# Optimization experiments

Hardware: AMD Instinct MI355X
Metric: run time of the kernel (lower is better)

## Reference

```python
import jax, jax.numpy as jnp
import numpy as np

N, E, C, MID = 20000, 320000, 16, 32
EPS = 1e-8

# ---- real Clebsch-Gordan (Q_J) matrices for degree pairs up to l=1, real-SH m-order (-l..l) i.e. (y,z,x) for l=1 ----

def _q_matrices():
    Q0 = np.eye(3, dtype=np.float32)[:, :, None] / np.sqrt(3.0)          # 1x1 -> J=0
    eps = np.zeros((3, 3, 3), dtype=np.float32)
    for (a, b, c_) in [(0, 1, 2), (1, 2, 0), (2, 0, 1)]:
        eps[a, b, c_] = 1.0
        eps[a, c_, b] = -1.0
    Q1 = eps / np.sqrt(2.0)                                               # 1x1 -> J=1 (cross product)
    Q2 = np.zeros((3, 3, 5), dtype=np.float32)                            # 1x1 -> J=2 (sym traceless)
    s2 = 1.0 / np.sqrt(2.0); s6 = 1.0 / np.sqrt(6.0)
    Q2[2, 0, 0] = Q2[0, 2, 0] = s2          # ~xy
    Q2[0, 1, 1] = Q2[1, 0, 1] = s2          # ~yz
    Q2[0, 0, 2] = -s6; Q2[1, 1, 2] = 2 * s6; Q2[2, 2, 2] = -s6  # ~(2z2-x2-y2)
    Q2[1, 2, 3] = Q2[2, 1, 3] = s2          # ~xz
    Q2[2, 2, 4] = s2; Q2[0, 0, 4] = -s2     # ~(x2-y2)
    return Q0, Q1, Q2

_Q0, _Q1, _Q2 = _q_matrices()


def _basis(u):
    """u: [E,3] unit edge directions -> basis tensors per (d_in,d_out) pair."""
    x, y, z = u[:, 0], u[:, 1], u[:, 2]
    Ep = u.shape[0]
    Y0 = jnp.full((Ep,), 0.28209479177387814, u.dtype)
    Y1 = 0.4886025119029199 * jnp.stack([y, z, x], -1)                    # m=-1,0,1
    Y2 = jnp.stack([1.0925484305920792 * x * y,
                    1.0925484305920792 * y * z,
                    0.31539156525252005 * (3.0 * z * z - 1.0),
                    1.0925484305920792 * x * z,
                    0.5462742152960396 * (x * x - y * y)], -1)
    b00 = Y0.reshape(Ep, 1, 1, 1, 1, 1)
    b01 = Y1.reshape(Ep, 1, 3, 1, 1, 1)
    b10 = Y1.reshape(Ep, 1, 1, 1, 3, 1)
    K0 = Y0[:, None, None] * jnp.asarray(_Q0[:, :, 0])
    K1 = jnp.einsum('em,abm->eab', Y1, jnp.asarray(_Q1))
    K2 = jnp.einsum('em,abm->eab', Y2, jnp.asarray(_Q2))
    b11 = jnp.stack([K0, K1, K2], -1).reshape(Ep, 1, 3, 1, 3, 3)          # num_freq=3 (J=0,1,2)
    return b00, b01, b10, b11


def _bn(x, g, b):  # BatchNorm1d, training-mode stats over edges, eps=1e-5
    mu = x.mean(0)
    var = ((x - mu) ** 2).mean(0)
    return (x - mu) * jax.lax.rsqrt(var + 1e-5) * g + b


def _hidden(feat, W1, b1, g1, be1, W2, b2, g2, be2):
    h = jax.nn.relu(_bn(feat @ W1 + b1, g1, be1))
    return jax.nn.relu(_bn(h @ W2 + b2, g2, be2))


def _kernel(Rflat, basis, nco, do_dim, nci, di_dim, nf):
    # RadialFunc output view: [E, nc_out, 1, nc_in, 1, num_freq]; contract freq with basis
    R = Rflat.reshape(-1, nco, 1, nci, 1, nf)
    k = (R * basis).sum(-1)                        # [E,nco,do_dim,nci,di_dim]
    return k.reshape(-1, nco * do_dim, nci * di_dim)


def _norm_bias(x, bias):  # GNormBias: relu(|x| + b) * phase
    n = jnp.sqrt((x * x).sum(-1, keepdims=True) + 1e-12)
    phase = x / jnp.maximum(n, EPS)
    return jax.nn.relu(n[..., 0] + bias)[..., None] * phase


def _forward(src, dst, pos, c, v, w,
             rW1, rb1, rg1, rbe1, rW2, rb2, rg2, rbe2,
             w3_a00, b3_a00, w3_a01, b3_a01, w3_a10, b3_a10, w3_a11, b3_a11,
             w3_b01, b3_b01, w3_b11, b3_b11,
             selfA0, selfA1, selfB1, nbias0, nbias1):
    n_nodes = c.shape[0]
    n_edges = src.shape[0]
    rel = pos[dst] - pos[src]
    r = jnp.sqrt((rel * rel).sum(-1, keepdims=True))                      # [E,1]
    u = rel / jnp.maximum(r, EPS)
    b00, b01, b10, b11 = _basis(u)
    feat = jnp.concatenate([w, r], -1)                                    # [E, edge_dim+1]
    # all 6 radial-net hiddens at once: [6,E,MID]
    H = jax.vmap(_hidden, in_axes=(None, 0, 0, 0, 0, 0, 0, 0, 0))(
        feat, rW1, rb1, rg1, rbe1, rW2, rb2, rg2, rbe2)
    deg = jax.ops.segment_sum(jnp.ones((n_edges,), feat.dtype), dst, num_segments=n_nodes)
    inv = (1.0 / jnp.maximum(deg, 1.0))[:, None, None]
    mask = (deg > 0).astype(feat.dtype)[:, None, None]
    # ---- layer A: in {0:1,1:1} -> mid {0:C,1:C} ----
    k00 = _kernel(H[0] @ w3_a00 + b3_a00, b00, C, 1, 1, 1, 1)             # [E,C,1]
    k01 = _kernel(H[1] @ w3_a01 + b3_a01, b01, C, 3, 1, 1, 1)             # [E,3C,1]
    k10 = _kernel(H[2] @ w3_a10 + b3_a10, b10, C, 1, 1, 3, 1)             # [E,C,3]
    k11 = _kernel(H[3] @ w3_a11 + b3_a11, b11, C, 3, 1, 3, 3)             # [E,3C,3]
    s0 = c[src].reshape(n_edges, 1, 1)
    s1 = v[src].reshape(n_edges, 3, 1)
    m0 = (k00 @ s0 + k10 @ s1).reshape(n_edges, C, 1)
    m1 = (k01 @ s0 + k11 @ s1).reshape(n_edges, C, 3)
    h0 = jax.ops.segment_sum(m0, dst, num_segments=n_nodes) * inv \
         + jnp.einsum('oi,nid->nod', selfA0[0], c) * mask
    h1 = jax.ops.segment_sum(m1, dst, num_segments=n_nodes) * inv \
         + jnp.einsum('oi,nid->nod', selfA1[0], v) * mask
    # ---- GNormBias on mid fiber ----
    h0 = _norm_bias(h0, nbias0)
    h1 = _norm_bias(h1, nbias1)
    # ---- layer B: mid {0:C,1:C} -> out {1:2} ----
    kb01 = _kernel(H[4] @ w3_b01 + b3_b01, b01, 2, 3, C, 1, 1)            # [E,6,C]
    kb11 = _kernel(H[5] @ w3_b11 + b3_b11, b11, 2, 3, C, 3, 3)            # [E,6,3C]
    t0 = h0[src]                                                          # [E,C,1]
    t1 = h1[src].reshape(n_edges, C * 3, 1)
    mB = (kb01 @ t0 + kb11 @ t1).reshape(n_edges, 2, 3)
    out = jax.ops.segment_sum(mB, dst, num_segments=n_nodes) * inv \
          + jnp.einsum('oi,nid->nod', selfB1[0], h1) * mask
    return out                                                            # [N,2,3]


def setup_inputs() -> dict:
    key = jax.random.key(0)
    ks = jax.random.split(key, 40)
    def rn(i, shape, scale=1.0):
        return jax.random.normal(ks[i], shape, jnp.float32) * scale
    K = 6
    sc = 1.0 / np.sqrt(MID)
    d = {}
    d['src'] = jax.random.randint(ks[0], (E,), 0, N)
    d['dst'] = jax.random.randint(ks[1], (E,), 0, N)
    d['pos'] = rn(2, (N, 3))
    d['c'] = rn(3, (N, 1, 1))
    d['v'] = rn(4, (N, 1, 3))
    d['w'] = rn(5, (E, 1))
    d['rW1'] = rn(6, (K, 2, MID), 1.0 / np.sqrt(2.0))
    d['rb1'] = jnp.zeros((K, MID), jnp.float32)
    d['rg1'] = jnp.ones((K, MID), jnp.float32)
    d['rbe1'] = jnp.zeros((K, MID), jnp.float32)
    d['rW2'] = rn(7, (K, MID, MID), sc)
    d['rb2'] = jnp.zeros((K, MID), jnp.float32)
    d['rg2'] = jnp.ones((K, MID), jnp.float32)
    d['rbe2'] = jnp.zeros((K, MID), jnp.float32)
    d['w3_a00'] = rn(8, (MID, C), sc);      d['b3_a00'] = jnp.zeros((C,), jnp.float32)
    d['w3_a01'] = rn(9, (MID, C), sc);      d['b3_a01'] = jnp.zeros((C,), jnp.float32)
    d['w3_a10'] = rn(10, (MID, C), sc);     d['b3_a10'] = jnp.zeros((C,), jnp.float32)
    d['w3_a11'] = rn(11, (MID, 3 * C), sc); d['b3_a11'] = jnp.zeros((3 * C,), jnp.float32)
    d['w3_b01'] = rn(12, (MID, 2 * C), sc); d['b3_b01'] = jnp.zeros((2 * C,), jnp.float32)
    d['w3_b11'] = rn(13, (MID, 6 * C), sc); d['b3_b11'] = jnp.zeros((6 * C,), jnp.float32)
    d['selfA0'] = rn(14, (1, C, 1))
    d['selfA1'] = rn(15, (1, C, 1))
    d['selfB1'] = rn(16, (1, 2, C), 1.0 / np.sqrt(C))
    d['nbias0'] = rn(17, (C,))
    d['nbias1'] = rn(18, (C,))
    return d


def reference(src, dst, pos, c, v, w,
              rW1, rb1, rg1, rbe1, rW2, rb2, rg2, rbe2,
              w3_a00, b3_a00, w3_a01, b3_a01, w3_a10, b3_a10, w3_a11, b3_a11,
              w3_b01, b3_b01, w3_b11, b3_b11,
              selfA0, selfA1, selfB1, nbias0, nbias1):
    return _forward(src, dst, pos, c, v, w,
                    rW1, rb1, rg1, rbe1, rW2, rb2, rg2, rbe2,
                    w3_a00, b3_a00, w3_a01, b3_a01, w3_a10, b3_a10, w3_a11, b3_a11,
                    w3_b01, b3_b01, w3_b11, b3_b11,
                    selfA0, selfA1, selfB1, nbias0, nbias1)
```

## Files before the change

kernel.cpp:

```cpp
#include <hip/hip_runtime.h>

#define NN 20000
#define NE 320000
#define CDIM 16
#define MID 32
#define EPSF 1e-8f

#define SCHED_FENCE() __builtin_amdgcn_sched_barrier(0)

#define OFF_DEGI   848
#define ZERO_WORDS 20848
#define OFF_ROWPTR 20848
#define OFF_CURSOR 40864
#define OFF_EORDER 60864
#define OFF_SRCS   380864
#define OFF_WSRT   700864
#define OFF_FW1A   1020864
#define OFF_FW1B   1021056
#define OFF_FC1    1021248
#define OFF_BN2A   1021440
#define OFF_FC2    1021632
#define OFF_FW2T   1021824
#define OFF_ECS    1027968
#define OFF_H0N    2307968
#define OFF_H1N    2627968
#define OFF_MSGA0  3587968
#define OFF_MSGA1  8707968
#define OFF_MSGB   24067968

#define Y0C   0.28209479177387814f
#define Y1C   0.4886025119029199f
#define Y2C1  1.0925484305920792f
#define Y2C2  0.31539156525252005f
#define Y2C3  0.5462742152960396f
#define S2C   0.7071067811865476f
#define S6C   0.4082482904638631f
#define K0C   0.16286750396763996f

__device__ __forceinline__ void atomAddD(double* p, double v) {
  unsafeAtomicAdd(p, v);
}

__device__ __forceinline__ void mlpH_lds(
    const float* __restrict__ a1, const float* __restrict__ b1v,
    const float* __restrict__ c1, const float* __restrict__ c2,
    const float* __restrict__ W2T, float we, float r, float* H) {
  float h[MID];
#pragma unroll
  for (int j4 = 0; j4 < 8; ++j4) {
    float4 av = ((const float4*)a1)[j4];
    float4 bv = ((const float4*)b1v)[j4];
    float4 cv = ((const float4*)c1)[j4];
    h[4 * j4 + 0] = fmaxf(fmaf(we, av.x, fmaf(r, bv.x, cv.x)), 0.0f);
    h[4 * j4 + 1] = fmaxf(fmaf(we, av.y, fmaf(r, bv.y, cv.y)), 0.0f);
    h[4 * j4 + 2] = fmaxf(fmaf(we, av.z, fmaf(r, bv.z, cv.z)), 0.0f);
    h[4 * j4 + 3] = fmaxf(fmaf(we, av.w, fmaf(r, bv.w, cv.w)), 0.0f);
  }
  SCHED_FENCE();
#pragma unroll
  for (int jg = 0; jg < 8; ++jg) {
#pragma unroll
// ... 32 lines not shown
    hA[4 * j4 + 1] = fmaxf(fmaf(weA, av.y, fmaf(rA, bv.y, cv.y)), 0.0f);
    hB[4 * j4 + 1] = fmaxf(fmaf(weB, av.y, fmaf(rB, bv.y, cv.y)), 0.0f);
    hA[4 * j4 + 2] = fmaxf(fmaf(weA, av.z, fmaf(rA, bv.z, cv.z)), 0.0f);
    hB[4 * j4 + 2] = fmaxf(fmaf(weB, av.z, fmaf(rB, bv.z, cv.z)), 0.0f);
    hA[4 * j4 + 3] = fmaxf(fmaf(weA, av.w, fmaf(rA, bv.w, cv.w)), 0.0f);
    hB[4 * j4 + 3] = fmaxf(fmaf(weB, av.w, fmaf(rB, bv.w, cv.w)), 0.0f);
  }
  SCHED_FENCE();
#pragma unroll
  for (int jg = 0; jg < 8; ++jg) {
#pragma unroll
    for (int jq = 0; jq < 4; ++jq) {
      const int j = jg * 4 + jq;
      float c2v = c2[j];
      float accA = c2v, accB = c2v;
      const float4* wp = (const float4*)(W2T + j * MID);
#pragma unroll
      for (int i4 = 0; i4 < 8; ++i4) {
        float4 wv = wp[i4];
        accA = fmaf(hA[4 * i4 + 0], wv.x, accA);
        accB = fmaf(hB[4 * i4 + 0], wv.x, accB);
        accA = fmaf(hA[4 * i4 + 1], wv.y, accA);
        accB = fmaf(hB[4 * i4 + 1], wv.y, accB);
        accA = fmaf(hA[4 * i4 + 2], wv.z, accA);
        accB = fmaf(hB[4 * i4 + 2], wv.z, accB);
        accA = fmaf(hA[4 * i4 + 3], wv.w, accA);
        accB = fmaf(hB[4 * i4 + 3], wv.w, accB);
      }
      HA[j] = fmaxf(accA, 0.0f);
      HB[j] = fmaxf(accB, 0.0f);
    }
    SCHED_FENCE();
  }
}

__global__ __launch_bounds__(256) void k_hist(
    const int* __restrict__ dst, float* __restrict__ ws) {
  int e = blockIdx.x * blockDim.x + threadIdx.x;
  if (e >= NE) return;
  atomicAdd((int*)ws + OFF_DEGI + dst[e], 1);
}

__global__ void k_scan(float* __restrict__ ws) {
  __shared__ int buf[256];
  __shared__ int carry;
  const int* degi = (const int*)ws + OFF_DEGI;
  int* rowptr = (int*)ws + OFF_ROWPTR;
  int* cursor = (int*)ws + OFF_CURSOR;
  int tid = threadIdx.x;
  if (tid == 0) carry = 0;
  __syncthreads();
  for (int base = 0; base < NN; base += 256) {
    int v = (base + tid < NN) ? degi[base + tid] : 0;
    buf[tid] = v;
    __syncthreads();
    for (int off = 1; off < 256; off <<= 1) {
      int t = buf[tid];
      int add = (tid >= off) ? buf[tid - off] : 0;
      __syncthreads();
      buf[tid] = t + add;
      __syncthreads();
    }
    int excl = buf[tid] - v;
    if (base + tid < NN) {
      rowptr[base + tid] = carry + excl;
      cursor[base + tid] = carry + excl;
// ... 57 lines not shown
    sred[2 * 4 + wid] = lww;
    sred[3 * 4 + wid] = lrr;
    sred[4 * 4 + wid] = lwr;
  }
  __syncthreads();
  if (threadIdx.x < 5) {
    double v = sred[threadIdx.x * 4 + 0] + sred[threadIdx.x * 4 + 1]
             + sred[threadIdx.x * 4 + 2] + sred[threadIdx.x * 4 + 3];
    atomAddD((double*)ws + threadIdx.x * 8, v);
  }
}

__global__ void k_fin1(const float* __restrict__ rW1, const float* __restrict__ rb1,
                       const float* __restrict__ rg1, const float* __restrict__ rbe1,
                       float* __restrict__ ws) {
  int t = threadIdx.x;
  int k = t >> 5, j = t & 31;
  const double* s1 = (const double*)ws;
  double Sw = s1[0], Sr = s1[8], Sww = s1[16], Srr = s1[24], Swr = s1[32];
  const double inv = 1.0 / (double)NE;
  double W0 = (double)rW1[k * 64 + j], W1 = (double)rW1[k * 64 + 32 + j];
  double b = (double)rb1[k * 32 + j];
  double mlin = (Sw * W0 + Sr * W1) * inv;
  double mu = mlin + b;
  double ex2 = (Sww * W0 * W0 + Srr * W1 * W1 + 2.0 * Swr * W0 * W1) * inv
             + 2.0 * b * mlin + b * b;
  double var = ex2 - mu * mu;
  double a = (double)rg1[k * 32 + j] / sqrt(var + 1e-5);
  ws[OFF_FW1A + t] = (float)(W0 * a);
  ws[OFF_FW1B + t] = (float)(W1 * a);
  ws[OFF_FC1 + t] = (float)((double)rbe1[k * 32 + j] - mlin * a);
}

__global__ __launch_bounds__(256) void k_stats2(
    const float* __restrict__ rW2, const float* __restrict__ rb2,
    float* __restrict__ ws) {
  const int k = blockIdx.y;
  const int j0 = blockIdx.z * 16;
  __shared__ __align__(16) float sW1a[32], sW1b[32], sc1[32];
  __shared__ __align__(16) float sW2c[512];
  __shared__ float sb2[16];
  __shared__ float sredf[2][16][4];
  int tid = threadIdx.x;
  if (tid < 32) {
    sW1a[tid] = ws[OFF_FW1A + k * 32 + tid];
    sW1b[tid] = ws[OFF_FW1B + k * 32 + tid];
    sc1[tid] = ws[OFF_FC1 + k * 32 + tid];
  }
  if (tid < 16) sb2[tid] = rb2[k * 32 + j0 + tid];
  for (int t = tid; t < 512; t += 256) {
    int jj = t >> 5, i = t & 31;
    sW2c[t] = rW2[k * 1024 + i * 32 + j0 + jj];
  }
  __syncthreads();
  const float4* ecs = (const float4*)(ws + OFF_ECS);
  const float* wsrt = ws + OFF_WSRT;
  float lsum[16], lsq[16];
#pragma unroll
  for (int jj = 0; jj < 16; ++jj) { lsum[jj] = 0.0f; lsq[jj] = 0.0f; }
  const int NP = NE / 2;
  for (int p = blockIdx.x * blockDim.x + tid; p < NP;
       p += gridDim.x * blockDim.x) {
    int e0 = 2 * p;
    float r0 = ecs[e0].x, r1 = ecs[e0 + 1].x;
    float w0 = wsrt[e0], w1 = wsrt[e0 + 1];
    float h0[MID], h1[MID];
// ... 44 lines not shown
#pragma unroll
    for (int d = 32; d >= 1; d >>= 1) {
      v1 += __shfl_xor(v1, d);
      v2 += __shfl_xor(v2, d);
    }
    if ((tid & 63) == 0) {
      sredf[0][jj][wid] = v1;
      sredf[1][jj][wid] = v2;
    }
  }
  __syncthreads();
  if (tid < 32) {
    int jj = tid & 15, which = tid >> 4;
    float v = sredf[which][jj][0] + sredf[which][jj][1]
            + sredf[which][jj][2] + sredf[which][jj][3];
    double* s2 = (double*)(ws + 80);
    atomAddD(s2 + k * 64 + which * 32 + j0 + jj, (double)v);
  }
}

__global__ void k_fin2(const float* __restrict__ rb2,
                       const float* __restrict__ rg2, const float* __restrict__ rbe2,
                       float* __restrict__ ws) {
  int t = threadIdx.x;
  int k = t >> 5, j = t & 31;
  const double* s2 = (const double*)(ws + 80);
  const double inv = 1.0 / (double)NE;
  double mu = s2[k * 64 + j] * inv;
  double ex2 = s2[k * 64 + 32 + j] * inv;
  double var = ex2 - mu * mu;
  double a = (double)rg2[t] / sqrt(var + 1e-5);
  ws[OFF_BN2A + t] = (float)a;
  ws[OFF_FC2 + t] = (float)((double)rbe2[t] + ((double)rb2[t] - mu) * a);
}

__global__ __launch_bounds__(256) void k_fold2(const float* __restrict__ rW2,
                                               float* __restrict__ ws) {
  int idx = blockIdx.x * blockDim.x + threadIdx.x;
  if (idx >= 6144) return;
  int k = idx >> 10, rem = idx & 1023;
  int j = rem >> 5, i = rem & 31;
  ws[OFF_FW2T + idx] = rW2[k * 1024 + i * 32 + j] * ws[OFF_BN2A + k * 32 + j];
}

__global__ __launch_bounds__(256) void k_passA0(
    const float* __restrict__ cI, const float* __restrict__ vI,
    const float* __restrict__ w00, const float* __restrict__ b00,
    const float* __restrict__ w10, const float* __restrict__ b10,
    float* __restrict__ ws) {
  __shared__ __align__(16) float sW1a[64], sW1b[64], sc1[64], sc2[64];
  __shared__ __align__(16) float sW2T[2048];
  __shared__ __align__(16) float sP00[512], sP10[512];
  __shared__ float sB00[16], sB10[16];
  int tid = threadIdx.x;
  if (tid < 32) {
    sW1a[tid] = ws[OFF_FW1A + tid];       sW1a[32 + tid] = ws[OFF_FW1A + 64 + tid];
    sW1b[tid] = ws[OFF_FW1B + tid];       sW1b[32 + tid] = ws[OFF_FW1B + 64 + tid];
    sc1[tid]  = ws[OFF_FC1 + tid];        sc1[32 + tid]  = ws[OFF_FC1 + 64 + tid];
    sc2[tid]  = ws[OFF_FC2 + tid];        sc2[32 + tid]  = ws[OFF_FC2 + 64 + tid];
  }
  for (int t = tid; t < 2048; t += 256) {
    sW2T[t] = ws[OFF_FW2T + ((t < 1024) ? t : (1024 + t))];
  }
  for (int t = tid; t < 512; t += 256) {
    int i = t >> 4, co = t & 15;
    sP00[co * 32 + i] = w00[t];
    sP10[co * 32 + i] = w10[t];
  }
  if (tid < 16) { sB00[tid] = b00[tid]; sB10[tid] = b10[tid]; }
  __syncthreads();

  const int* srcs = (const int*)ws + OFF_SRCS;
  const float* wsrt = ws + OFF_WSRT;
  const float4* ecs = (const float4*)(ws + OFF_ECS);
  int t = blockIdx.x * blockDim.x + tid;
// ... 177 lines not shown
    const float* __restrict__ selfA0, const float* __restrict__ selfA1,
    const float* __restrict__ nbias0, const float* __restrict__ nbias1,
    float* __restrict__ ws) {
  int idx = blockIdx.x * blockDim.x + threadIdx.x;
  if (idx >= NN * CDIM) return;
  int n = idx >> 4, co = idx & 15;
  const int* rowptr = (const int*)ws + OFF_ROWPTR;
  int r0 = rowptr[n], r1 = rowptr[n + 1];
  const float* mA0 = ws + OFF_MSGA0;
  const float* mA1 = ws + OFF_MSGA1 + (co >> 2) * (NE * 12) + (co & 3) * 3;
  float x0 = 0.0f, xa = 0.0f, xb = 0.0f, xc = 0.0f;
  for (int row = r0; row < r1; ++row) {
    x0 += mA0[row * 16 + co];
    xa += mA1[row * 12 + 0];
    xb += mA1[row * 12 + 1];
    xc += mA1[row * 12 + 2];
  }
  float dg = (float)(r1 - r0);
  float iv = 1.0f / fmaxf(dg, 1.0f);
  float mk = dg > 0.0f ? 1.0f : 0.0f;
  x0 = x0 * iv + selfA0[co] * cI[n] * mk;
  float n0 = sqrtf(x0 * x0 + 1e-12f);
  ws[OFF_H0N + idx] = fmaxf(n0 + nbias0[co], 0.0f) * (x0 / fmaxf(n0, EPSF));
  xa = xa * iv + selfA1[co] * vI[3 * n + 0] * mk;
  xb = xb * iv + selfA1[co] * vI[3 * n + 1] * mk;
  xc = xc * iv + selfA1[co] * vI[3 * n + 2] * mk;
  float nv = sqrtf(xa * xa + xb * xb + xc * xc + 1e-12f);
  float sc = fmaxf(nv + nbias1[co], 0.0f) / fmaxf(nv, EPSF);
  ws[OFF_H1N + idx * 3 + 0] = xa * sc;
  ws[OFF_H1N + idx * 3 + 1] = xb * sc;
  ws[OFF_H1N + idx * 3 + 2] = xc * sc;
}

__global__ __launch_bounds__(256) void k_passB(
    const float* __restrict__ wb01, const float* __restrict__ bb01,
    const float* __restrict__ wb11, const float* __restrict__ bb11,
    float* __restrict__ ws) {
  __shared__ __align__(16) float sW1a[64], sW1b[64], sc1[64], sc2[64];
  __shared__ __align__(16) float sW2T[2048];
  __shared__ __align__(16) float sPB01[1024];
  __shared__ __align__(16) float sPB11[3072];
  __shared__ float sBB01[32];
  __shared__ float sBB11[96];
  int tid = threadIdx.x;
  if (tid < 64) {
    sW1a[tid] = ws[OFF_FW1A + 128 + tid];
    sW1b[tid] = ws[OFF_FW1B + 128 + tid];
    sc1[tid] = ws[OFF_FC1 + 128 + tid];
    sc2[tid] = ws[OFF_FC2 + 128 + tid];
  }
  for (int t = tid; t < 2048; t += 256) sW2T[t] = ws[OFF_FW2T + 4096 + t];
  for (int t = tid; t < 1024; t += 256) {
    int i = t >> 5, c = t & 31;
    int o = c >> 4, ci = c & 15;
    sPB01[(ci * 2 + o) * 32 + i] = wb01[t];
  }
  for (int t = tid; t < 3072; t += 256) {
    int i = t / 96, c = t - i * 96;
    int o = c / 48, rem = c - o * 48;
    int ci = rem / 3, f = rem - ci * 3;
    sPB11[(ci * 6 + o * 3 + f) * 32 + i] = wb11[t];
  }
  if (tid < 32) {
    int o = tid >> 4, ci = tid & 15;
    sBB01[ci * 2 + o] = bb01[tid];
  }
// ... 141 lines not shown
      }
    }
  }
}

__global__ __launch_bounds__(256) void k_nodeB(
    const float* __restrict__ selfB1, float* __restrict__ out,
    const float* __restrict__ ws) {
  int idx = blockIdx.x * blockDim.x + threadIdx.x;
  if (idx >= NN * 6) return;
  int n = idx / 6;
  int q = idx - n * 6;
  int o = q / 3, a = q - o * 3;
  const int* rowptr = (const int*)ws + OFF_ROWPTR;
  int r0 = rowptr[n], r1 = rowptr[n + 1];
  const float* msgB = ws + OFF_MSGB;
  int col = o * 4 + a;
  float sum = 0.0f;
  for (int row = r0; row < r1; ++row) sum += msgB[row * 8 + col];
  float dg = (float)(r1 - r0);
  float iv = 1.0f / fmaxf(dg, 1.0f);
  float mk = dg > 0.0f ? 1.0f : 0.0f;
  const float* h1p = ws + OFF_H1N + n * CDIM * 3;
  float self = 0.0f;
#pragma unroll
  for (int ci = 0; ci < CDIM; ++ci)
    self = fmaf(selfB1[o * CDIM + ci], h1p[ci * 3 + a], self);
  out[idx] = sum * iv + self * mk;
}

extern "C" void kernel_launch(void* const* d_in, const int* in_sizes, int n_in,
                              void* d_out, int out_size, void* d_ws, size_t ws_size,
                              hipStream_t stream) {
  (void)in_sizes; (void)n_in; (void)out_size; (void)ws_size;
  const int* src = (const int*)d_in[0];
  const int* dst = (const int*)d_in[1];
  const float* pos = (const float*)d_in[2];
  const float* cI = (const float*)d_in[3];
  const float* vI = (const float*)d_in[4];
  const float* w = (const float*)d_in[5];
  const float* rW1 = (const float*)d_in[6];
  const float* rb1 = (const float*)d_in[7];
  const float* rg1 = (const float*)d_in[8];
  const float* rbe1 = (const float*)d_in[9];
  const float* rW2 = (const float*)d_in[10];
  const float* rb2 = (const float*)d_in[11];
  const float* rg2 = (const float*)d_in[12];
  const float* rbe2 = (const float*)d_in[13];
  const float* w3_a00 = (const float*)d_in[14];
  const float* b3_a00 = (const float*)d_in[15];
  const float* w3_a01 = (const float*)d_in[16];
  const float* b3_a01 = (const float*)d_in[17];
  const float* w3_a10 = (const float*)d_in[18];
  const float* b3_a10 = (const float*)d_in[19];
  const float* w3_a11 = (const float*)d_in[20];
  const float* b3_a11 = (const float*)d_in[21];
  const float* w3_b01 = (const float*)d_in[22];
  const float* b3_b01 = (const float*)d_in[23];
  const float* w3_b11 = (const float*)d_in[24];
  const float* b3_b11 = (const float*)d_in[25];
  const float* selfA0 = (const float*)d_in[26];
  const float* selfA1 = (const float*)d_in[27];
  const float* selfB1 = (const float*)d_in[28];
  const float* nbias0 = (const float*)d_in[29];
  const float* nbias1 = (const float*)d_in[30];
  float* ws = (float*)d_ws;
  float* out = (float*)d_out;

  hipMemsetAsync(d_ws, 0, (size_t)ZERO_WORDS * 4, stream);

  k_hist<<<1250, 256, 0, stream>>>(dst, ws);
  k_scan<<<1, 256, 0, stream>>>(ws);
  k_scatter<<<1250, 256, 0, stream>>>(dst, ws);
  k_geo<<<1250, 256, 0, stream>>>(src, dst, pos, w, ws);
  k_fin1<<<1, 192, 0, stream>>>(rW1, rb1, rg1, rbe1, ws);
  k_stats2<<<dim3(256, 6, 2), 256, 0, stream>>>(rW2, rb2, ws);
  k_fin2<<<1, 192, 0, stream>>>(rb2, rg2, rbe2, ws);
  k_fold2<<<24, 256, 0, stream>>>(rW2, ws);
  k_passA0<<<1250, 256, 0, stream>>>(cI, vI, w3_a00, b3_a00, w3_a10, b3_a10, ws);
  k_passA1<<<1250, 256, 0, stream>>>(cI, vI, w3_a01, b3_a01, w3_a11, b3_a11, ws);
  k_nodeA<<<1250, 256, 0, stream>>>(cI, vI, selfA0, selfA1, nbias0, nbias1, ws);
  k_passB<<<625, 256, 0, stream>>>(w3_b01, b3_b01, w3_b11, b3_b11, ws);
  k_nodeB<<<469, 256, 0, stream>>>(selfB1, out, ws);
}
```

Measured before the change: 540.2 us.

## Materialize radial MLP pre-activations once and reuse across stats and message passes

Adds a k_mlp kernel that computes the second-layer pre-BN activations for all six radial MLPs per edge and stores them in workspace (about 61M floats). The BN2 statistics pass and the message passes then read these stored values and apply only the BN affine and ReLU, instead of recomputing the 32x32 matmul several times. This trades repeated matmul compute for roughly 245 MB of extra global writes and reads. The new path runs only when the workspace is large enough, otherwise it falls back to the old kernels.

```diff
diff --git a/kernel.cpp b/kernel.cpp
--- a/kernel.cpp
+++ b/kernel.cpp
@@ -12,6 +12,7 @@
 #define ZERO_WORDS 20848
 #define OFF_ROWPTR 20848
 #define OFF_CURSOR 40864
+#define OFF_CC2    40864
 #define OFF_EORDER 60864
 #define OFF_SRCS   380864
 #define OFF_WSRT   700864
@@ -27,6 +28,8 @@
 #define OFF_MSGA0  3587968
 #define OFF_MSGA1  8707968
 #define OFF_MSGB   24067968
+#define OFF_PRE    26627968
+#define WS_WORDS_NEEDED 88067968ULL
 
 #define Y0C   0.28209479177387814f
 #define Y1C   0.4886025119029199f
@@ -125,6 +128,22 @@
     }
     SCHED_FENCE();
   }
+}
+
+__device__ __forceinline__ void loadH_P(
+    const float4* __restrict__ pp, const float* __restrict__ a2,
+    const float* __restrict__ cc, float* H) {
+#pragma unroll
+  for (int j4 = 0; j4 < 8; ++j4) {
+    float4 v = pp[j4];
+    float4 av = ((const float4*)a2)[j4];
+    float4 cv = ((const float4*)cc)[j4];
+    H[4 * j4 + 0] = fmaxf(fmaf(av.x, v.x, cv.x), 0.0f);
+    H[4 * j4 + 1] = fmaxf(fmaf(av.y, v.y, cv.y), 0.0f);
+    H[4 * j4 + 2] = fmaxf(fmaf(av.z, v.z, cv.z), 0.0f);
+    H[4 * j4 + 3] = fmaxf(fmaf(av.w, v.w, cv.w), 0.0f);
+  }
+  SCHED_FENCE();
 }
 
 __global__ __launch_bounds__(256) void k_hist(
@@ -248,6 +267,157 @@
   ws[OFF_FC1 + t] = (float)((double)rbe1[k * 32 + j] - mlin * a);
 }
 
+__global__ __launch_bounds__(256) void k_mlp(
+    const float* __restrict__ rW2, const float* __restrict__ rb2,
+    float* __restrict__ ws) {
+  __shared__ __align__(16) float sW1a[192], sW1b[192], sc1[192], sB2[192];
+  __shared__ __align__(16) float sW2T6[6144];
+  int tid = threadIdx.x;
+  if (tid < 192) {
+    sW1a[tid] = ws[OFF_FW1A + tid];
+    sW1b[tid] = ws[OFF_FW1B + tid];
+    sc1[tid] = ws[OFF_FC1 + tid];
+    sB2[tid] = rb2[tid];
+  }
+  for (int t2 = tid; t2 < 6144; t2 += 256) {
+    int k = t2 >> 10, rem = t2 & 1023;
+    int j = rem >> 5, i = rem & 31;
+    sW2T6[t2] = rW2[k * 1024 + i * 32 + j];
+  }
+  __syncthreads();
+
+  const float* wsrt = ws + OFF_WSRT;
+  const float4* ecs = (const float4*)(ws + OFF_ECS);
+  int t = blockIdx.x * blockDim.x + tid;
+  if (t >= NE) return;
+  float we = wsrt[t];
+  float r = ecs[t].x;
+
+#pragma unroll 1
+  for (int k = 0; k < 6; ++k) {
+    const float* a1 = sW1a + k * 32;
+    const float* b1 = sW1b + k * 32;
+    const float* c1 = sc1 + k * 32;
+    const float* b2 = sB2 + k * 32;
+    const float* w2 = sW2T6 + k * 1024;
+    float h[MID];
+#pragma unroll
+    for (int j4 = 0; j4 < 8; ++j4) {
+      float4 av = ((const float4*)a1)[j4];
+      float4 bv = ((const float4*)b1)[j4];
+      float4 cv = ((const float4*)c1)[j4];
+      h[4 * j4 + 0] = fmaxf(fmaf(we, av.x, fmaf(r, bv.x, cv.x)), 0.0f);
+      h[4 * j4 + 1] = fmaxf(fmaf(we, av.y, fmaf(r, bv.y, cv.y)), 0.0f);
+      h[4 * j4 + 2] = fmaxf(fmaf(we, av.z, fmaf(r, bv.z, cv.z)), 0.0f);
+      h[4 * j4 + 3] = fmaxf(fmaf(we, av.w, fmaf(r, bv.w, cv.w)), 0.0f);
+    }
+    SCHED_FENCE();
+    float4* pp = (float4*)(ws + OFF_PRE) + (size_t)k * (NE * 8) + (size_t)t * 8;
+#pragma unroll
+    for (int jg = 0; jg < 8; ++jg) {
+      float q0, q1, q2, q3;
+      {
+        float acc = b2[jg * 4 + 0];
+        const float4* wp = (const float4*)(w2 + (jg * 4 + 0) * 32);
+#pragma unroll
+        for (int i4 = 0; i4 < 8; ++i4) {
+          float4 wv = wp[i4];
+          acc = fmaf(h[4 * i4 + 0], wv.x, acc);
+          acc = fmaf(h[4 * i4 + 1], wv.y, acc);
+          acc = fmaf(h[4 * i4 + 2], wv.z, acc);
+          acc = fmaf(h[4 * i4 + 3], wv.w, acc);
+        }
+        q0 = acc;
+      }
+      {
+        float acc = b2[jg * 4 + 1];
+        const float4* wp = (const float4*)(w2 + (jg * 4 + 1) * 32);
+#pragma unroll
+        for (int i4 = 0; i4 < 8; ++i4) {
+          float4 wv = wp[i4];
+          acc = fmaf(h[4 * i4 + 0], wv.x, acc);
+          acc = fmaf(h[4 * i4 + 1], wv.y, acc);
+          acc = fmaf(h[4 * i4 + 2], wv.z, acc);
+          acc = fmaf(h[4 * i4 + 3], wv.w, acc);
+        }
+        q1 = acc;
+      }
+      {
+        float acc = b2[jg * 4 + 2];
+        const float4* wp = (const float4*)(w2 + (jg * 4 + 2) * 32);
+#pragma unroll
+        for (int i4 = 0; i4 < 8; ++i4) {
+          float4 wv = wp[i4];
+          acc = fmaf(h[4 * i4 + 0], wv.x, acc);
+          acc = fmaf(h[4 * i4 + 1], wv.y, acc);
+          acc = fmaf(h[4 * i4 + 2], wv.z, acc);
+          acc = fmaf(h[4 * i4 + 3], wv.w, acc);
+        }
+        q2 = acc;
+      }
+      {
+        float acc = b2[jg * 4 + 3];
+        const float4* wp = (const float4*)(w2 + (jg * 4 + 3) * 32);
+#pragma unroll
+        for (int i4 = 0; i4 < 8; ++i4) {
+          float4 wv = wp[i4];
+          acc = fmaf(h[4 * i4 + 0], wv.x, acc);
+          acc = fmaf(h[4 * i4 + 1], wv.y, acc);
+          acc = fmaf(h[4 * i4 + 2], wv.z, acc);
+          acc = fmaf(h[4 * i4 + 3], wv.w, acc);
+        }
+        q3 = acc;
+      }
+      pp[jg] = make_float4(q0, q1, q2, q3);
+      SCHED_FENCE();
+    }
+  }
+}
+
+__global__ __launch_bounds__(256) void k_stats2P(float* __restrict__ ws) {
+  const int k = blockIdx.y;
+  __shared__ float sredf[2][32][4];
+  int tid = threadIdx.x;
+  float ls[32], lq[32];
+#pragma unroll
+  for (int j = 0; j < 32; ++j) { ls[j] = 0.0f; lq[j] = 0.0f; }
+  const float4* Pk = (const float4*)(ws + OFF_PRE) + (size_t)k * (NE * 8);
+  for (int t = blockIdx.x * blockDim.x + tid; t < NE;
+       t += gridDim.x * blockDim.x) {
+    const float4* pp = Pk + (size_t)t * 8;
+#pragma unroll
+    for (int j4 = 0; j4 < 8; ++j4) {
+      float4 v = pp[j4];
+      ls[4 * j4 + 0] += v.x; lq[4 * j4 + 0] = fmaf(v.x, v.x, lq[4 * j4 + 0]);
+      ls[4 * j4 + 1] += v.y; lq[4 * j4 + 1] = fmaf(v.y, v.y, lq[4 * j4 + 1]);
+      ls[4 * j4 + 2] += v.z; lq[4 * j4 + 2] = fmaf(v.z, v.z, lq[4 * j4 + 2]);
+      ls[4 * j4 + 3] += v.w; lq[4 * j4 + 3] = fmaf(v.w, v.w, lq[4 * j4 + 3]);
+    }
+  }
+  int wid = tid >> 6;
+#pragma unroll
+  for (int j = 0; j < 32; ++j) {
+    float v1 = ls[j], v2 = lq[j];
+#pragma unroll
+    for (int d = 32; d >= 1; d >>= 1) {
+      v1 += __shfl_xor(v1, d);
+      v2 += __shfl_xor(v2, d);
+    }
+    if ((tid & 63) == 0) {
+      sredf[0][j][wid] = v1;
+      sredf[1][j][wid] = v2;
+    }
+  }
+  __syncthreads();
+  if (tid < 64) {
+    int j = tid & 31, which = tid >> 5;
+    float v = sredf[which][j][0] + sredf[which][j][1]
+            + sredf[which][j][2] + sredf[which][j][3];
+    double* s2 = (double*)(ws + 80);
+    atomAddD(s2 + k * 64 + which * 32 + j, (double)v);
+  }
+}
+
 __global__ __launch_bounds__(256) void k_stats2(
     const float* __restrict__ rW2, const float* __restrict__ rb2,
     float* __restrict__ ws) {
@@ -358,6 +528,7 @@
   double a = (double)rg2[t] / sqrt(var + 1e-5);
   ws[OFF_BN2A + t] = (float)a;
   ws[OFF_FC2 + t] = (float)((double)rbe2[t] + ((double)rb2[t] - mu) * a);
+  ws[OFF_CC2 + t] = (float)((double)rbe2[t] - mu * a);
 }
 
 __global__ __launch_bounds__(256) void k_fold2(const float* __restrict__ rW2,
@@ -367,6 +538,202 @@
   int k = idx >> 10, rem = idx & 1023;
   int j = rem >> 5, i = rem & 31;
   ws[OFF_FW2T + idx] = rW2[k * 1024 + i * 32 + j] * ws[OFF_BN2A + k * 32 + j];
+}
+
+__global__ __launch_bounds__(256) void k_passA0P(
+    const float* __restrict__ cI, const float* __restrict__ vI,
+    const float* __restrict__ w00, const float* __restrict__ b00,
+    const float* __restrict__ w10, const float* __restrict__ b10,
+    float* __restrict__ ws) {
+  __shared__ __align__(16) float sA2a[32], sCCa[32], sA2b[32], sCCb[32];
+  __shared__ __align__(16) float sP00[512], sP10[512];
+  __shared__ float sB00[16], sB10[16];
+  int tid = threadIdx.x;
+  if (tid < 32) {
+    sA2a[tid] = ws[OFF_BN2A + tid];
+    sCCa[tid] = ws[OFF_CC2 + tid];
+    sA2b[tid] = ws[OFF_BN2A + 64 + tid];
+    sCCb[tid] = ws[OFF_CC2 + 64 + tid];
+  }
+  for (int t2 = tid; t2 < 512; t2 += 256) {
+    int i = t2 >> 4, co = t2 & 15;
+    sP00[co * 32 + i] = w00[t2];
+    sP10[co * 32 + i] = w10[t2];
+  }
+  if (tid < 16) { sB00[tid] = b00[tid]; sB10[tid] = b10[tid]; }
+  __syncthreads();
+
+  const int* srcs = (const int*)ws + OFF_SRCS;
+  const float4* ecs = (const float4*)(ws + OFF_ECS);
+  int t = blockIdx.x * blockDim.x + tid;
+  if (t >= NE) return;
+  int s = srcs[t];
+  float4 E = ecs[t];
+  float cs = cI[s];
+  float v0 = vI[3 * s + 0], v1 = vI[3 * s + 1], v2 = vI[3 * s + 2];
+  float dY1v = Y1C * (E.z * v0 + E.w * v1 + E.y * v2);
+
+  float H[MID], m0[CDIM];
+  loadH_P((const float4*)(ws + OFF_PRE) + (size_t)t * 8, sA2a, sCCa, H);
+  float f0 = Y0C * cs;
+#pragma unroll
+  for (int cg = 0; cg < 4; ++cg) {
+#pragma unroll
+    for (int cq = 0; cq < 4; ++cq) {
+      const int co = cg * 4 + cq;
+      float a = sB00[co];
+      const float4* wp = (const float4*)(sP00 + co * 32);
+#pragma unroll
+      for (int i4 = 0; i4 < 8; ++i4) {
+        float4 wv = wp[i4];
+        a = fmaf(H[4 * i4 + 0], wv.x, a);
+        a = fmaf(H[4 * i4 + 1], wv.y, a);
+        a = fmaf(H[4 * i4 + 2], wv.z, a);
+        a = fmaf(H[4 * i4 + 3], wv.w, a);
+      }
+      m0[co] = a * f0;
+    }
+    SCHED_FENCE();
+  }
+  loadH_P((const float4*)(ws + OFF_PRE) + (size_t)2 * (NE * 8) + (size_t)t * 8,
+          sA2b, sCCb, H);
+#pragma unroll
+  for (int cg = 0; cg < 4; ++cg) {
+#pragma unroll
+    for (int cq = 0; cq < 4; ++cq) {
+      const int co = cg * 4 + cq;
+      float a = sB10[co];
+      const float4* wp = (const float4*)(sP10 + co * 32);
+#pragma unroll
+      for (int i4 = 0; i4 < 8; ++i4) {
+        float4 wv = wp[i4];
+        a = fmaf(H[4 * i4 + 0], wv.x, a);
+        a = fmaf(H[4 * i4 + 1], wv.y, a);
+        a = fmaf(H[4 * i4 + 2], wv.z, a);
+        a = fmaf(H[4 * i4 + 3], wv.w, a);
+      }
+      m0[co] = fmaf(a, dY1v, m0[co]);
+    }
+    SCHED_FENCE();
+  }
+  float4* mp = (float4*)(ws + OFF_MSGA0) + t * 4;
+#pragma unroll
+  for (int q = 0; q < 4; ++q)
+    mp[q] = make_float4(m0[4 * q], m0[4 * q + 1], m0[4 * q + 2], m0[4 * q + 3]);
+}
+
+__global__ __launch_bounds__(256) void k_passA1P(
+    const float* __restrict__ cI, const float* __restrict__ vI,
+    const float* __restrict__ w01, const float* __restrict__ b01,
+    const float* __restrict__ w11, const float* __restrict__ b11,
+    float* __restrict__ ws) {
+  __shared__ __align__(16) float sA2a[32], sCCa[32], sA2b[32], sCCb[32];
+  __shared__ __align__(16) float sP01[512], sP11[1536];
+  __shared__ float sB01[16], sB11[48];
+  int tid = threadIdx.x;
+  if (tid < 32) {
+    sA2a[tid] = ws[OFF_BN2A + 32 + tid];
+    sCCa[tid] = ws[OFF_CC2 + 32 + tid];
+    sA2b[tid] = ws[OFF_BN2A + 96 + tid];
+    sCCb[tid] = ws[OFF_CC2 + 96 + tid];
+  }
+  for (int t2 = tid; t2 < 512; t2 += 256) {
+    int i = t2 >> 4, co = t2 & 15;
+    sP01[co * 32 + i] = w01[t2];
+  }
+  for (int t2 = tid; t2 < 1536; t2 += 256) {
+    int i = t2 / 48, c = t2 - i * 48;
+    sP11[c * 32 + i] = w11[t2];
+  }
+  if (tid < 16) sB01[tid] = b01[tid];
+  if (tid < 48) sB11[tid] = b11[tid];
+  __syncthreads();
+
+  const int* srcs = (const int*)ws + OFF_SRCS;
+  const float4* ecs = (const float4*)(ws + OFF_ECS);
+  int t = blockIdx.x * blockDim.x + tid;
+  if (t >= NE) return;
+  int s = srcs[t];
+  float4 E = ecs[t];
+  float cs = cI[s];
+
+  float H[MID];
+  float ra[16];
+  loadH_P((const float4*)(ws + OFF_PRE) + (size_t)1 * (NE * 8) + (size_t)t * 8,
+          sA2a, sCCa, H);
+#pragma unroll
+  for (int cg = 0; cg < 4; ++cg) {
+#pragma unroll
+    for (int cq = 0; cq < 4; ++cq) {
+      const int co = cg * 4 + cq;
+      float a = sB01[co];
+      const float4* wp = (const float4*)(sP01 + co * 32);
+#pragma unroll
+      for (int i4 = 0; i4 < 8; ++i4) {
+        float4 wv = wp[i4];
+        a = fmaf(H[4 * i4 + 0], wv.x, a);
+        a = fmaf(H[4 * i4 + 1], wv.y, a);
+        a = fmaf(H[4 * i4 + 2], wv.z, a);
+        a = fmaf(H[4 * i4 + 3], wv.w, a);
+      }
+      ra[co] = a;
+    }
+    SCHED_FENCE();
+  }
+  loadH_P((const float4*)(ws + OFF_PRE) + (size_t)3 * (NE * 8) + (size_t)t * 8,
+          sA2b, sCCb, H);
+  float y10 = Y1C * E.z, y11 = Y1C * E.w, y12 = Y1C * E.y;
+  float KV[3][3];
+  {
+    float ux = E.y, uy = E.z, uz = E.w;
+    float y20 = Y2C1 * ux * uy, y21 = Y2C1 * uy * uz;
+    float y22 = Y2C2 * (3.0f * uz * uz - 1.0f);
+    float y23 = Y2C1 * ux * uz, y24 = Y2C3 * (ux * ux - uy * uy);
+    float S00 = -S6C * y22 - S2C * y24;
+    float S11 = 2.0f * S6C * y22;
+    float S22 = -S6C * y22 + S2C * y24;
+    float S01 = S2C * y21, S02 = S2C * y20, S12 = S2C * y23;
+    float v0 = vI[3 * s + 0], v1 = vI[3 * s + 1], v2 = vI[3 * s + 2];
+    KV[0][0] = K0C * v0; KV[0][1] = K0C * v1; KV[0][2] = K0C * v2;
+    KV[1][0] = S2C * (y12 * v1 - y11 * v2);
+    KV[1][1] = S2C * (y10 * v2 - y12 * v0);
+    KV[1][2] = S2C * (y11 * v0 - y10 * v1);
+    KV[2][0] = S00 * v0 + S01 * v1 + S02 * v2;
+    KV[2][1] = S01 * v0 + S11 * v1 + S12 * v2;
+    KV[2][2] = S02 * v0 + S12 * v1 + S22 * v2;
+  }
+  float cy0 = cs * y10, cy1 = cs * y11, cy2 = cs * y12;
+#pragma unroll 1
+  for (int g = 0; g < 4; ++g) {
+    float a[12];
+#pragma unroll
+    for (int q = 0; q < 4; ++q) {
+      int co = g * 4 + q;
+      float R0 = sB11[co * 3 + 0], R1 = sB11[co * 3 + 1], R2 = sB11[co * 3 + 2];
+      const float4* p0 = (const float4*)(sP11 + (co * 3 + 0) * 32);
+      const float4* p1 = (const float4*)(sP11 + (co * 3 + 1) * 32);
+      const float4* p2 = (const float4*)(sP11 + (co * 3 + 2) * 32);
+#pragma unroll
+      for (int i4 = 0; i4 < 8; ++i4) {
+        float4 w0v = p0[i4], w1v = p1[i4], w2v = p2[i4];
+        float h0 = H[4 * i4 + 0], h1 = H[4 * i4 + 1];
+        float h2 = H[4 * i4 + 2], h3 = H[4 * i4 + 3];
+        R0 = fmaf(h0, w0v.x, R0); R1 = fmaf(h0, w1v.x, R1); R2 = fmaf(h0, w2v.x, R2);
+        R0 = fmaf(h1, w0v.y, R0); R1 = fmaf(h1, w1v.y, R1); R2 = fmaf(h1, w2v.y, R2);
+        R0 = fmaf(h2, w0v.z, R0); R1 = fmaf(h2, w1v.z, R1); R2 = fmaf(h2, w2v.z, R2);
+        R0 = fmaf(h3, w0v.w, R0); R1 = fmaf(h3, w1v.w, R1); R2 = fmaf(h3, w2v.w, R2);
+      }
+      float r_ = ra[co];
+      a[q * 3 + 0] = fmaf(r_, cy0, R0 * KV[0][0] + R1 * KV[1][0] + R2 * KV[2][0]);
+      a[q * 3 + 1] = fmaf(r_, cy1, R0 * KV[0][1] + R1 * KV[1][1] + R2 * KV[2][1]);
+      a[q * 3 + 2] = fmaf(r_, cy2, R0 * KV[0][2] + R1 * KV[1][2] + R2 * KV[2][2]);
+    }
+    float4* mp = (float4*)(ws + OFF_MSGA1 + g * (NE * 12)) + t * 3;
+    mp[0] = make_float4(a[0], a[1], a[2], a[3]);
+    mp[1] = make_float4(a[4], a[5], a[6], a[7]);
+    mp[2] = make_float4(a[8], a[9], a[10], a[11]);
+    SCHED_FENCE();
+  }
 }
 
 __global__ __launch_bounds__(256) void k_passA0(
@@ -610,6 +977,186 @@
   ws[OFF_H1N + idx * 3 + 2] = xc * sc;
 }
 
+__global__ __launch_bounds__(256) void k_passBP(
+    const float* __restrict__ wb01, const float* __restrict__ bb01,
+    const float* __restrict__ wb11, const float* __restrict__ bb11,
+    float* __restrict__ ws) {
+  __shared__ __align__(16) float sA2a[32], sCCa[32], sA2b[32], sCCb[32];
+  __shared__ __align__(16) float sPB01[1024];
+  __shared__ __align__(16) float sPB11[3072];
+  __shared__ float sBB01[32];
+  __shared__ float sBB11[96];
+  int tid = threadIdx.x;
+  if (tid < 32) {
+    sA2a[tid] = ws[OFF_BN2A + 128 + tid];
+    sCCa[tid] = ws[OFF_CC2 + 128 + tid];
+    sA2b[tid] = ws[OFF_BN2A + 160 + tid];
+    sCCb[tid] = ws[OFF_CC2 + 160 + tid];
+  }
+  for (int t = tid; t < 1024; t += 256) {
+    int i = t >> 5, c = t & 31;
+    int o = c >> 4, ci = c & 15;
+    sPB01[(ci * 2 + o) * 32 + i] = wb01[t];
+  }
+  for (int t = tid; t < 3072; t += 256) {
+    int i = t / 96, c = t - i * 96;
+    int o = c / 48, rem = c - o * 48;
+    int ci = rem / 3, f = rem - ci * 3;
+    sPB11[(ci * 6 + o * 3 + f) * 32 + i] = wb11[t];
+  }
+  if (tid < 32) {
+    int o = tid >> 4, ci = tid & 15;
+    sBB01[ci * 2 + o] = bb01[tid];
+  }
+  if (tid < 96) {
+    int o = tid / 48, rem = tid - o * 48;
+    int ci = rem / 3, f = rem - ci * 3;
+    sBB11[ci * 6 + o * 3 + f] = bb11[tid];
+  }
+  __syncthreads();
+
+  const int* srcs = (const int*)ws + OFF_SRCS;
+  const float4* ecs = (const float4*)(ws + OFF_ECS);
+  const int NP = NE / 2;
+  int p = blockIdx.x * blockDim.x + tid;
+  if (p >= NP) return;
+  {
+    int tA = 2 * p, tB = 2 * p + 1;
+    int sA = srcs[tA], sB_ = srcs[tB];
+    float4 EA = ecs[tA], EB = ecs[tB];
+
+    float HA[MID], HB[MID];
+    loadH_P((const float4*)(ws + OFF_PRE) + (size_t)4 * (NE * 8) + (size_t)tA * 8,
+            sA2a, sCCa, HA);
+    loadH_P((const float4*)(ws + OFF_PRE) + (size_t)4 * (NE * 8) + (size_t)tB * 8,
+            sA2a, sCCa, HB);
+    const float* h0pA = ws + OFF_H0N + sA * CDIM;
+    const float* h0pB = ws + OFF_H0N + sB_ * CDIM;
+    float A0A = 0.0f, A1A = 0.0f, A0B = 0.0f, A1B = 0.0f;
+#pragma unroll 1
+    for (int ci = 0; ci < CDIM; ++ci) {
+      float bA = h0pA[ci], bB = h0pB[ci];
+      float R0A = sBB01[ci * 2 + 0], R1A = sBB01[ci * 2 + 1];
+      float R0B = R0A, R1B = R1A;
+      const float4* p0 = (const float4*)(sPB01 + (ci * 2 + 0) * 32);
+      const float4* p1 = (const float4*)(sPB01 + (ci * 2 + 1) * 32);
+#pragma unroll
+      for (int i4 = 0; i4 < 8; ++i4) {
+        float4 w0v = p0[i4], w1v = p1[i4];
+        float hA0 = HA[4 * i4 + 0], hB0 = HB[4 * i4 + 0];
+        float hA1 = HA[4 * i4 + 1], hB1 = HB[4 * i4 + 1];
+        float hA2 = HA[4 * i4 + 2], hB2 = HB[4 * i4 + 2];
+        float hA3 = HA[4 * i4 + 3], hB3 = HB[4 * i4 + 3];
+        R0A = fmaf(hA0, w0v.x, R0A); R0B = fmaf(hB0, w0v.x, R0B);
+        R1A = fmaf(hA0, w1v.x, R1A); R1B = fmaf(hB0, w1v.x, R1B);
+        R0A = fmaf(hA1, w0v.y, R0A); R0B = fmaf(hB1, w0v.y, R0B);
+        R1A = fmaf(hA1, w1v.y, R1A); R1B = fmaf(hB1, w1v.y, R1B);
+        R0A = fmaf(hA2, w0v.z, R0A); R0B = fmaf(hB2, w0v.z, R0B);
+        R1A = fmaf(hA2, w1v.z, R1A); R1B = fmaf(hB2, w1v.z, R1B);
+        R0A = fmaf(hA3, w0v.w, R0A); R0B = fmaf(hB3, w0v.w, R0B);
+        R1A = fmaf(hA3, w1v.w, R1A); R1B = fmaf(hB3, w1v.w, R1B);
+      }
+      A0A = fmaf(R0A, bA, A0A); A1A = fmaf(R1A, bA, A1A);
+      A0B = fmaf(R0B, bB, A0B); A1B = fmaf(R1B, bB, A1B);
+      SCHED_FENCE();
+    }
+    loadH_P((const float4*)(ws + OFF_PRE) + (size_t)5 * (NE * 8) + (size_t)tA * 8,
+            sA2b, sCCb, HA);
+    loadH_P((const float4*)(ws + OFF_PRE) + (size_t)5 * (NE * 8) + (size_t)tB * 8,
+            sA2b, sCCb, HB);
+    const float* h1pA = ws + OFF_H1N + sA * CDIM * 3;
+    const float* h1pB = ws + OFF_H1N + sB_ * CDIM * 3;
+    float GA[6][3], GB[6][3];
+#pragma unroll
+    for (int of = 0; of < 6; ++of) {
+      GA[of][0] = 0.0f; GA[of][1] = 0.0f; GA[of][2] = 0.0f;
+      GB[of][0] = 0.0f; GB[of][1] = 0.0f; GB[of][2] = 0.0f;
+    }
+#pragma unroll 1
+    for (int ci = 0; ci < CDIM; ++ci) {
+      float bA0 = h1pA[ci * 3 + 0], bA1 = h1pA[ci * 3 + 1], bA2 = h1pA[ci * 3 + 2];
+      float bB0 = h1pB[ci * 3 + 0], bB1 = h1pB[ci * 3 + 1], bB2 = h1pB[ci * 3 + 2];
+#pragma unroll
+      for (int of = 0; of < 6; ++of) {
+        float RA = sBB11[ci * 6 + of];
+        float RB = RA;
+        const float4* wp = (const float4*)(sPB11 + (ci * 6 + of) * 32);
+#pragma unroll
+        for (int i4 = 0; i4 < 8; ++i4) {
+          float4 wv = wp[i4];
+          RA = fmaf(HA[4 * i4 + 0], wv.x, RA);
+          RB = fmaf(HB[4 * i4 + 0], wv.x, RB);
+          RA = fmaf(HA[4 * i4 + 1], wv.y, RA);
+          RB = fmaf(HB[4 * i4 + 1], wv.y, RB);
+          RA = fmaf(HA[4 * i4 + 2], wv.z, RA);
+          RB = fmaf(HB[4 * i4 + 2], wv.z, RB);
+          RA = fmaf(HA[4 * i4 + 3], wv.w, RA);
+          RB = fmaf(HB[4 * i4 + 3], wv.w, RB);
+        }
+        GA[of][0] = fmaf(RA, bA0, GA[of][0]);
+        GA[of][1] = fmaf(RA, bA1, GA[of][1]);
+        GA[of][2] = fmaf(RA, bA2, GA[of][2]);
+        GB[of][0] = fmaf(RB, bB0, GB[of][0]);
+        GB[of][1] = fmaf(RB, bB1, GB[of][1]);
+        GB[of][2] = fmaf(RB, bB2, GB[of][2]);
+      }
+      SCHED_FENCE();
+    }
+    {
+      float ux = EA.y, uy = EA.z, uz = EA.w;
+      float y10 = Y1C * uy, y11 = Y1C * uz, y12 = Y1C * ux;
+      float y20 = Y2C1 * ux * uy, y21 = Y2C1 * uy * uz;
+      float y22 = Y2C2 * (3.0f * uz * uz - 1.0f);
+      float y23 = Y2C1 * ux * uz, y24 = Y2C3 * (ux * ux - uy * uy);
+      float S00 = -S6C * y22 - S2C * y24;
+      float S11 = 2.0f * S6C * y22;
+      float S22 = -S6C * y22 + S2C * y24;
+      float S01 = S2C * y21, S02 = S2C * y20, S12 = S2C * y23;
+      float4* mp = (float4*)(ws + OFF_MSGB) + tA * 2;
+#pragma unroll
+      for (int o = 0; o < 2; ++o) {
+        float Ao = (o == 0) ? A0A : A1A;
+        float m0 = Ao * y10 + K0C * GA[o * 3 + 0][0]
+                 + S2C * (y12 * GA[o * 3 + 1][1] - y11 * GA[o * 3 + 1][2])
+                 + S00 * GA[o * 3 + 2][0] + S01 * GA[o * 3 + 2][1] + S02 * GA[o * 3 + 2][2];
+        float m1 = Ao * y11 + K0C * GA[o * 3 + 0][1]
+                 + S2C * (y10 * GA[o * 3 + 1][2] - y12 * GA[o * 3 + 1][0])
+                 + S01 * GA[o * 3 + 2][0] + S11 * GA[o * 3 + 2][1] + S12 * GA[o * 3 + 2][2];
+        float m2 = Ao * y12 + K0C * GA[o * 3 + 0][2]
+                 + S2C * (y11 * GA[o * 3 + 1][0] - y10 * GA[o * 3 + 1][1])
+                 + S02 * GA[o * 3 + 2][0] + S12 * GA[o * 3 + 2][1] + S22 * GA[o * 3 + 2][2];
+        mp[o] = make_float4(m0, m1, m2, 0.0f);
+      }
+    }
+    {
+      float ux = EB.y, uy = EB.z, uz = EB.w;
+      float y10 = Y1C * uy, y11 = Y1C * uz, y12 = Y1C * ux;
+      float y20 = Y2C1 * ux * uy, y21 = Y2C1 * uy * uz;
+      float y22 = Y2C2 * (3.0f * uz * uz - 1.0f);
+      float y23 = Y2C1 * ux * uz, y24 = Y2C3 * (ux * ux - uy * uy);
+      float S00 = -S6C * y22 - S2C * y24;
+      float S11 = 2.0f * S6C * y22;
+      float S22 = -S6C * y22 + S2C * y24;
+      float S01 = S2C * y21, S02 = S2C * y20, S12 = S2C * y23;
+      float4* mp = (float4*)(ws + OFF_MSGB) + tB * 2;
+#pragma unroll
+      for (int o = 0; o < 2; ++o) {
+        float Ao = (o == 0) ? A0B : A1B;
+        float m0 = Ao * y10 + K0C * GB[o * 3 + 0][0]
+                 + S2C * (y12 * GB[o * 3 + 1][1] - y11 * GB[o * 3 + 1][2])
+                 + S00 * GB[o * 3 + 2][0] + S01 * GB[o * 3 + 2][1] + S02 * GB[o * 3 + 2][2];
+        float m1 = Ao * y11 + K0C * GB[o * 3 + 0][1]
+                 + S2C * (y10 * GB[o * 3 + 1][2] - y12 * GB[o * 3 + 1][0])
+                 + S01 * GB[o * 3 + 2][0] + S11 * GB[o * 3 + 2][1] + S12 * GB[o * 3 + 2][2];
+        float m2 = Ao * y12 + K0C * GB[o * 3 + 0][2]
+                 + S2C * (y11 * GB[o * 3 + 1][0] - y10 * GB[o * 3 + 1][1])
+                 + S02 * GB[o * 3 + 2][0] + S12 * GB[o * 3 + 2][1] + S22 * GB[o * 3 + 2][2];
+        mp[o] = make_float4(m0, m1, m2, 0.0f);
+      }
+    }
+  }
+}
+
 __global__ __launch_bounds__(256) void k_passB(
     const float* __restrict__ wb01, const float* __restrict__ bb01,
     const float* __restrict__ wb11, const float* __restrict__ bb11,
@@ -817,7 +1364,7 @@
 extern "C" void kernel_launch(void* const* d_in, const int* in_sizes, int n_in,
                               void* d_out, int out_size, void* d_ws, size_t ws_size,
                               hipStream_t stream) {
-  (void)in_sizes; (void)n_in; (void)out_size; (void)ws_size;
+  (void)in_sizes; (void)n_in; (void)out_size;
   const int* src = (const int*)d_in[0];
   const int* dst = (const int*)d_in[1];
   const float* pos = (const float*)d_in[2];
@@ -852,6 +1399,8 @@
   float* ws = (float*)d_ws;
   float* out = (float*)d_out;
 
+  const bool bigws = (ws_size >= WS_WORDS_NEEDED * 4ULL);
+
   hipMemsetAsync(d_ws, 0, (size_t)ZERO_WORDS * 4, stream);
 
   k_hist<<<1250, 256, 0, stream>>>(dst, ws);
@@ -859,12 +1408,23 @@
   k_scatter<<<1250, 256, 0, stream>>>(dst, ws);
   k_geo<<<1250, 256, 0, stream>>>(src, dst, pos, w, ws);
   k_fin1<<<1, 192, 0, stream>>>(rW1, rb1, rg1, rbe1, ws);
-  k_stats2<<<dim3(256, 6, 2), 256, 0, stream>>>(rW2, rb2, ws);
-  k_fin2<<<1, 192, 0, stream>>>(rb2, rg2, rbe2, ws);
-  k_fold2<<<24, 256, 0, stream>>>(rW2, ws);
-  k_passA0<<<1250, 256, 0, stream>>>(cI, vI, w3_a00, b3_a00, w3_a10, b3_a10, ws);
-  k_passA1<<<1250, 256, 0, stream>>>(cI, vI, w3_a01, b3_a01, w3_a11, b3_a11, ws);
-  k_nodeA<<<1250, 256, 0, stream>>>(cI, vI, selfA0, selfA1, nbias0, nbias1, ws);
-  k_passB<<<625, 256, 0, stream>>>(w3_b01, b3_b01, w3_b11, b3_b11, ws);
+
+  if (bigws) {
+    k_mlp<<<1250, 256, 0, stream>>>(rW2, rb2, ws);
+    k_stats2P<<<dim3(256, 6), 256, 0, stream>>>(ws);
+    k_fin2<<<1, 192, 0, stream>>>(rb2, rg2, rbe2, ws);
+    k_passA0P<<<1250, 256, 0, stream>>>(cI, vI, w3_a00, b3_a00, w3_a10, b3_a10, ws);
+    k_passA1P<<<1250, 256, 0, stream>>>(cI, vI, w3_a01, b3_a01, w3_a11, b3_a11, ws);
+    k_nodeA<<<1250, 256, 0, stream>>>(cI, vI, selfA0, selfA1, nbias0, nbias1, ws);
+    k_passBP<<<625, 256, 0, stream>>>(w3_b01, b3_b01, w3_b11, b3_b11, ws);
+  } else {
+    k_stats2<<<dim3(256, 6, 2), 256, 0, stream>>>(rW2, rb2, ws);
+    k_fin2<<<1, 192, 0, stream>>>(rb2, rg2, rbe2, ws);
+    k_fold2<<<24, 256, 0, stream>>>(rW2, ws);
+    k_passA0<<<1250, 256, 0, stream>>>(cI, vI, w3_a00, b3_a00, w3_a10, b3_a10, ws);
+    k_passA1<<<1250, 256, 0, stream>>>(cI, vI, w3_a01, b3_a01, w3_a11, b3_a11, ws);
+    k_nodeA<<<1250, 256, 0, stream>>>(cI, vI, selfA0, selfA1, nbias0, nbias1, ws);
+    k_passB<<<625, 256, 0, stream>>>(w3_b01, b3_b01, w3_b11, b3_b11, ws);
+  }
   k_nodeB<<<469, 256, 0, stream>>>(selfB1, out, ws);
 }
```

After: 541.1 us. No clear change (+0.2%).
